# Kernel optimization log

Hardware: AMD Instinct MI355X
Metric: run time of the kernel (lower is better)

Reference implementation:

```python
import jax, jax.numpy as jnp
import numpy as np

NUM_NET = 2
V = 100000
D = 128
B = 4096
K = 5
NS = 10
HYP1 = 0.1
HYP2 = 0.1
HYP3 = 0.1


def setup_inputs() -> dict:
    key = jax.random.key(0)
    ks = jax.random.split(key, 10)
    ri = lambda k, shape: jax.random.randint(k, shape, 0, V, dtype=jnp.int32)
    return {
        "node_tables": jax.random.normal(ks[0], (NUM_NET, V, D), jnp.float32) * 0.1,
        "neigh_tables": jax.random.normal(ks[1], (NUM_NET, V, D), jnp.float32) * 0.1,
        "nodes_idx": ri(ks[2], (NUM_NET, B)),
        "neigh_idx": ri(ks[3], (NUM_NET, B, K)),
        "role_idx": ri(ks[4], (NUM_NET, NUM_NET, B)),
        "neg_main": ri(ks[5], (NUM_NET, B, K * NS)),
        "neg_node": ri(ks[6], (NUM_NET, NUM_NET, B, 1 * NS)),
        "neg_cross": ri(ks[7], (NUM_NET, NUM_NET, B, K * NS)),
        "neg_role": ri(ks[8], (NUM_NET, NUM_NET, B, 1 * NS)),
    }


def _pos_loss(ctx, node):
    # ctx: (B, M, D), node: (B, D) -> mean over all logsigmoid(ctx . node)
    return jax.nn.log_sigmoid(jnp.einsum("bmd,bd->bm", ctx, node)).mean()


def _neg_loss(neg_ctx, node):
    # ctx embeddings are negated: logsigmoid(-(neg . node)), sum over samples, mean over batch
    return jax.nn.log_sigmoid(-jnp.einsum("bmd,bd->bm", neg_ctx, node)).sum(axis=1).mean()


def reference(node_tables, neigh_tables, nodes_idx, neigh_idx, role_idx,
              neg_main, neg_node, neg_cross, neg_role):
    cost = []
    for i in range(NUM_NET):
        node_emb = node_tables[i][nodes_idx[i]]          # (B, D)
        # main SGNS loss on view i (neigh tables)
        neigh_emb = neigh_tables[i][neigh_idx[i]]        # (B, K, D)
        c = _pos_loss(neigh_emb, node_emb) + _neg_loss(neigh_tables[i][neg_main[i]], node_emb)
        cost.append(c)
        # cross-view node alignment (node tables of j at same node indices)
        for j in range(NUM_NET):
            if j != i:
                ctx = node_tables[j][nodes_idx[i]][:, None, :]   # (B, 1, D)
                c = _pos_loss(ctx, node_emb) + _neg_loss(node_tables[j][neg_node[i, j]], node_emb)
                cost.append(HYP1 * c)
        # cross-view neighbor loss (neigh tables of j at view-i neighbor indices)
        for j in range(NUM_NET):
            if j != i:
                ctx = neigh_tables[j][neigh_idx[i]]              # (B, K, D)
                c = _pos_loss(ctx, node_emb) + _neg_loss(neigh_tables[j][neg_cross[i, j]], node_emb)
                cost.append(HYP2 * c)
        # role-based loss (node tables of all j at role indices)
        for j in range(NUM_NET):
            ctx = node_tables[j][role_idx[i, j]][:, None, :]     # (B, 1, D)
            c = _pos_loss(ctx, node_emb) + _neg_loss(node_tables[j][neg_role[i, j]], node_emb)
            cost.append(HYP3 * c)
    total = cost[0]
    for c in cost[1:]:
        total = total + c
    return -total / len(cost)
```

## Files before the change

kernel.cpp:

```cpp
#include <hip/hip_runtime.h>

#define NUM_NET 2
#define V 100000
#define D 128
#define B 4096
#define K 5
#define NS 10

#define W_MAIN_POS (1.0f/20480.0f)
#define W_INV_B    (1.0f/4096.0f)
#define HYP_B      (0.1f/4096.0f)
#define HYP2_BK    (0.1f/20480.0f)


__global__ __launch_bounds__(256, 8) void rmne_main(
    const float* __restrict__ node_tables,
    const float* __restrict__ neigh_tables,
    const int*   __restrict__ nodes_idx,
    const int*   __restrict__ neigh_idx,
    const int*   __restrict__ role_idx,
    const int*   __restrict__ neg_main,
    const int*   __restrict__ neg_node,
    const int*   __restrict__ neg_cross,
    const int*   __restrict__ neg_role,
    float*       __restrict__ out)
{
    const int tid  = threadIdx.x;
    const int lane = tid & 63;
    const int wave = tid >> 6;
    const int unit = blockIdx.x * 4 + wave;
    const int i = unit >> 12;
    const int b = unit & (B - 1);
    const int j = 1 - i;

    int pk[3];
    #pragma unroll
    for (int s = 0; s < 3; ++s) {
        int d = lane + 64 * s;
        int idx = 0, tab = 0, code = 7;
        if      (d <   5) { idx = neigh_idx[(i*B + b)*K + d];              tab = 2 + i; code = 0; }
        else if (d <  55) { idx = neg_main[(i*B + b)*50 + (d-5)];          tab = 2 + i; code = 3; }
        else if (d <  56) { idx = nodes_idx[i*B + b];                      tab = j;     code = 4; }
        else if (d <  66) { idx = neg_node[((i*2+j)*B + b)*NS + (d-56)];   tab = j;     code = 5; }
        else if (d <  71) { idx = neigh_idx[(i*B + b)*K + (d-66)];         tab = 2 + j; code = 6; }
        else if (d < 121) { idx = neg_cross[((i*2+j)*B + b)*50 + (d-71)];  tab = 2 + j; code = 5; }
        else if (d < 122) { idx = role_idx[(i*2+0)*B + b];                 tab = 0;     code = 4; }
        else if (d < 132) { idx = neg_role[((i*2+0)*B + b)*NS + (d-122)];  tab = 0;     code = 5; }
        else if (d < 133) { idx = role_idx[(i*2+1)*B + b];                 tab = 1;     code = 4; }
        else if (d < 143) { idx = neg_role[((i*2+1)*B + b)*NS + (d-133)];  tab = 1;     code = 5; }
        pk[s] = idx | (tab << 20) | (code << 22);
    }

    const int l16     = lane & 15;
    const int quarter = lane >> 4;
    const int nrow    = nodes_idx[i*B + b];
    const float4* nrp = (const float4*)(node_tables + ((size_t)i*V + (size_t)nrow)*D) + l16*2;
    const float4 ne0 = nrp[0];
    const float4 ne1 = nrp[1];

    float acc = 0.0f;

    int e_cur, e_mid, e_nxt;
    float4 cc0, cc1, m0, m1, n0, n1;

    auto rowload = [&](int e, float4& r0, float4& r1) {
        int idx = e & 0xFFFFF;
        int tab = (e >> 20) & 3;
        const float* base = (tab & 2) ? neigh_tables : node_tables;
        const float4* row = (const float4*)(base + ((size_t)(tab & 1)*V + (size_t)idx)*D) + l16*2;
        r0 = row[0];
        r1 = row[1];
    };

    auto compute = [&]() {
        float pp = ne0.x*cc0.x + ne0.y*cc0.y + ne0.z*cc0.z + ne0.w*cc0.w
                 + ne1.x*cc1.x + ne1.y*cc1.y + ne1.z*cc1.z + ne1.w*cc1.w;
        pp += __shfl_xor(pp, 1, 64);
        pp += __shfl_xor(pp, 2, 64);
        pp += __shfl_xor(pp, 4, 64);
        pp += __shfl_xor(pp, 8, 64);
        int code = (e_cur >> 22) & 7;
        float mag = (code == 0) ? W_MAIN_POS
                  : (code == 3) ? W_INV_B
                  : (code == 6) ? HYP2_BK
                  : (code == 7) ? 0.0f
                  : HYP_B;
        float x  = (code & 1) ? -pp : pp;
        float ls = fminf(x, 0.0f) - __logf(1.0f + __expf(-fabsf(x)));
        acc += mag * ls;
    };

    auto rotate = [&]() {
        e_cur = e_mid; cc0 = m0; cc1 = m1;
        e_mid = e_nxt; m0  = n0; m1  = n1;
    };

    e_cur = __shfl(pk[0], quarter, 64);
    rowload(e_cur, cc0, cc1);
    e_mid = __shfl(pk[0], 4 + quarter, 64);
    rowload(e_mid, m0, m1);

    auto step = [&](int tn, int slotpk) {
        e_nxt = __shfl(slotpk, (4*tn + quarter) & 63, 64);
        rowload(e_nxt, n0, n1);
        compute();
        rotate();
    };

    #pragma unroll 4
    for (int tn = 2;  tn < 16; ++tn) step(tn, pk[0]);
    #pragma unroll 4
    for (int tn = 16; tn < 32; ++tn) step(tn, pk[1]);
    #pragma unroll
    for (int tn = 32; tn < 36; ++tn) step(tn, pk[2]);

    compute();
    e_cur = e_mid; cc0 = m0; cc1 = m1;
    compute();

    acc += __shfl_xor(acc, 16, 64);
    acc += __shfl_xor(acc, 32, 64);

    __shared__ float wsum[4];
    if (lane == 0) wsum[wave] = acc;
    __syncthreads();
    if (tid == 0) {
        float s = wsum[0] + wsum[1] + wsum[2] + wsum[3];
        atomicAdd(out, s * (-1.0f / 10.0f));
    }
}

extern "C" void kernel_launch(void* const* d_in, const int* in_sizes, int n_in,
                              void* d_out, int out_size, void* d_ws, size_t ws_size,
                              hipStream_t stream) {
    const float* node_tables  = (const float*)d_in[0];
    const float* neigh_tables = (const float*)d_in[1];
    const int*   nodes_idx    = (const int*)d_in[2];
    const int*   neigh_idx    = (const int*)d_in[3];
    const int*   role_idx     = (const int*)d_in[4];
    const int*   neg_main     = (const int*)d_in[5];
    const int*   neg_node     = (const int*)d_in[6];
    const int*   neg_cross    = (const int*)d_in[7];
    const int*   neg_role     = (const int*)d_in[8];
    float* out = (float*)d_out;

    hipMemsetAsync(out, 0, sizeof(float), stream);
    rmne_main<<<2048, 256, 0, stream>>>(node_tables, neigh_tables, nodes_idx, neigh_idx,
                                        role_idx, neg_main, neg_node, neg_cross, neg_role, out);
}
```

Before: 285.6 us.

## Gather embedding rows via direct global-to-LDS loads with double buffering

```diff
diff --git a/kernel.cpp b/kernel.cpp
--- a/kernel.cpp
+++ b/kernel.cpp
@@ -12,8 +12,31 @@
 #define HYP_B      (0.1f/4096.0f)
 #define HYP2_BK    (0.1f/20480.0f)
 
+#define GLOBAL_AS __attribute__((address_space(1)))
+#define LDS_AS    __attribute__((address_space(3)))
 
-__global__ __launch_bounds__(256, 8) void rmne_main(
+__device__ __forceinline__ void gl_lds16(const float* g, float* l) {
+    __builtin_amdgcn_global_load_lds((const GLOBAL_AS unsigned int*)g,
+                                     (LDS_AS unsigned int*)l, 16, 0, 0);
+}
+
+__device__ __forceinline__ float dot8(float4 a0, float4 a1, float4 b0, float4 b1) {
+    return a0.x*b0.x + a0.y*b0.y + a0.z*b0.z + a0.w*b0.w
+         + a1.x*b1.x + a1.y*b1.y + a1.z*b1.z + a1.w*b1.w;
+}
+
+__device__ __forceinline__ float wlogsig(float pp, int code) {
+    float mag = (code == 0) ? W_MAIN_POS
+              : (code == 3) ? W_INV_B
+              : (code == 6) ? HYP2_BK
+              : (code == 7) ? 0.0f
+              : HYP_B;
+    float x  = (code & 1) ? -pp : pp;
+    float ls = fminf(x, 0.0f) - __logf(1.0f + __expf(-fabsf(x)));
+    return mag * ls;
+}
+
+__global__ __launch_bounds__(256) void rmne_main(
     const float* __restrict__ node_tables,
     const float* __restrict__ neigh_tables,
     const int*   __restrict__ nodes_idx,
@@ -25,6 +48,8 @@
     const int*   __restrict__ neg_role,
     float*       __restrict__ out)
 {
+    __shared__ float lbuf[4][2][1024];
+
     const int tid  = threadIdx.x;
     const int lane = tid & 63;
     const int wave = tid >> 6;
@@ -54,69 +79,53 @@
     const int l16     = lane & 15;
     const int quarter = lane >> 4;
     const int nrow    = nodes_idx[i*B + b];
-    const float4* nrp = (const float4*)(node_tables + ((size_t)i*V + (size_t)nrow)*D) + l16*2;
-    const float4 ne0 = nrp[0];
-    const float4 ne1 = nrp[1];
+    const float4* nep = (const float4*)(node_tables + ((size_t)i*V + (size_t)nrow)*D) + l16*2;
+    const float4 ne0 = nep[0];
+    const float4 ne1 = nep[1];
 
     float acc = 0.0f;
 
-    int e_cur, e_mid, e_nxt;
-    float4 cc0, cc1, m0, m1, n0, n1;
-
-    auto rowload = [&](int e, float4& r0, float4& r1) {
-        int idx = e & 0xFFFFF;
-        int tab = (e >> 20) & 3;
-        const float* base = (tab & 2) ? neigh_tables : node_tables;
-        const float4* row = (const float4*)(base + ((size_t)(tab & 1)*V + (size_t)idx)*D) + l16*2;
-        r0 = row[0];
-        r1 = row[1];
+    auto issue = [&](int bb, int parity) {
+        float* Lb = &lbuf[wave][parity][0];
+        #pragma unroll
+        for (int t = 0; t < 4; ++t) {
+            int e = 8*bb + 2*t + (lane >> 5);
+            int p = __shfl(pk[bb >> 3], e & 63, 64);
+            int idx = p & 0xFFFFF;
+            int tab = (p >> 20) & 3;
+            const float* base = (tab & 2) ? neigh_tables : node_tables;
+            const float* g = base + ((size_t)(tab & 1)*V + (size_t)idx)*D + (lane & 31)*4;
+            gl_lds16(g, Lb + t*256);
+        }
     };
 
-    auto compute = [&]() {
-        float pp = ne0.x*cc0.x + ne0.y*cc0.y + ne0.z*cc0.z + ne0.w*cc0.w
-                 + ne1.x*cc1.x + ne1.y*cc1.y + ne1.z*cc1.z + ne1.w*cc1.w;
-        pp += __shfl_xor(pp, 1, 64);
-        pp += __shfl_xor(pp, 2, 64);
-        pp += __shfl_xor(pp, 4, 64);
-        pp += __shfl_xor(pp, 8, 64);
-        int code = (e_cur >> 22) & 7;
-        float mag = (code == 0) ? W_MAIN_POS
-                  : (code == 3) ? W_INV_B
-                  : (code == 6) ? HYP2_BK
-                  : (code == 7) ? 0.0f
-                  : HYP_B;
-        float x  = (code & 1) ? -pp : pp;
-        float ls = fminf(x, 0.0f) - __logf(1.0f + __expf(-fabsf(x)));
-        acc += mag * ls;
+    auto compute = [&](int bb, int parity) {
+        const float* Lb = &lbuf[wave][parity][0];
+        #pragma unroll
+        for (int it = 0; it < 2; ++it) {
+            int ein = 4*it + quarter;
+            int p = __shfl(pk[bb >> 3], (8*bb + ein) & 63, 64);
+            const float4* r = (const float4*)(Lb + ein*128 + l16*8);
+            float4 c0 = r[0];
+            float4 c1 = r[1];
+            float pp = dot8(ne0, ne1, c0, c1);
+            pp += __shfl_xor(pp, 1, 64);
+            pp += __shfl_xor(pp, 2, 64);
+            pp += __shfl_xor(pp, 4, 64);
+            pp += __shfl_xor(pp, 8, 64);
+            acc += wlogsig(pp, (p >> 22) & 7);
+        }
     };
 
-    auto rotate = [&]() {
-        e_cur = e_mid; cc0 = m0; cc1 = m1;
-        e_mid = e_nxt; m0  = n0; m1  = n1;
-    };
-
-    e_cur = __shfl(pk[0], quarter, 64);
-    rowload(e_cur, cc0, cc1);
-    e_mid = __shfl(pk[0], 4 + quarter, 64);
-    rowload(e_mid, m0, m1);
-
-    auto step = [&](int tn, int slotpk) {
-        e_nxt = __shfl(slotpk, (4*tn + quarter) & 63, 64);
-        rowload(e_nxt, n0, n1);
-        compute();
-        rotate();
-    };
-
-    #pragma unroll 4
-    for (int tn = 2;  tn < 16; ++tn) step(tn, pk[0]);
-    #pragma unroll 4
-    for (int tn = 16; tn < 32; ++tn) step(tn, pk[1]);
+    issue(0, 0);
     #pragma unroll
-    for (int tn = 32; tn < 36; ++tn) step(tn, pk[2]);
-
-    compute();
-    e_cur = e_mid; cc0 = m0; cc1 = m1;
-    compute();
+    for (int bb = 0; bb < 17; ++bb) {
+        issue(bb + 1, (bb + 1) & 1);
+        asm volatile("s_waitcnt vmcnt(4)" ::: "memory");
+        compute(bb, bb & 1);
+    }
+    asm volatile("s_waitcnt vmcnt(0)" ::: "memory");
+    compute(17, 1);
 
     acc += __shfl_xor(acc, 16, 64);
     acc += __shfl_xor(acc, 32, 64);
```

New measurement: 295.3 us. +3.4%, slower.
